# Performance work log

Hardware: AMD Instinct MI355X
Metric: run time of the kernel (lower is better)

Reference implementation:

```python
import jax, jax.numpy as jnp
import numpy as np


def _per_qubit_unitary(theta):
    # theta: [L, Nq, 3] float -> combined per-qubit 2x2 unitary [Nq, 2, 2] complex64
    # Circuit applies, for each layer l (l=0 first): RZ(theta[l,i,0]) -> RY(theta[l,i,1]) -> RZ(theta[l,i,2])
    half = theta.astype(jnp.float32) * 0.5

    def rz(p):  # p: [Nq] -> [Nq,2,2]
        e = jnp.exp(-1j * p)  # complex64
        z = jnp.zeros_like(e)
        return jnp.stack([jnp.stack([e, z], -1), jnp.stack([z, jnp.conj(e)], -1)], -2)

    def ry(p):  # p: [Nq] -> [Nq,2,2]
        c, s = jnp.cos(p), jnp.sin(p)
        return jnp.stack([jnp.stack([c, -s], -1), jnp.stack([s, c], -1)], -2).astype(jnp.complex64)

    n_layers, n_qubits = theta.shape[0], theta.shape[1]
    U = jnp.broadcast_to(jnp.eye(2, dtype=jnp.complex64), (n_qubits, 2, 2))
    for l in range(n_layers):  # small fixed layer loop
        Ul = rz(half[l, :, 2]) @ ry(half[l, :, 1]) @ rz(half[l, :, 0])
        U = Ul @ U
    return U


def _vqc_state(angles, theta):
    # angles: [B,S,Nq]; theta: [L,Nq,3] -> real part of 2^Nq state vector, [B,S,2^Nq]
    half = angles * 0.5
    # RY(a)|0> = cos(a/2)|0> + sin(a/2)|1>
    v = jnp.stack([jnp.cos(half), jnp.sin(half)], -1).astype(jnp.complex64)  # [B,S,Nq,2]
    U = _per_qubit_unitary(theta)  # [Nq,2,2]
    v = jnp.einsum('nij,bsnj->bsni', U, v)  # apply layered single-qubit unitaries
    # Kron across qubits; PennyLane wire 0 is most significant -> left-to-right kron
    state = v[:, :, 0, :]  # [B,S,2]
    n_qubits = v.shape[2]
    for q in range(1, n_qubits):  # small fixed qubit loop
        state = (state[..., :, None] * v[:, :, q][..., None, :])
        state = state.reshape(state.shape[0], state.shape[1], -1)
    return jnp.real(state)


def setup_inputs() -> dict:
    key = jax.random.key(0)
    k0, k1, k2, k3 = jax.random.split(key, 4)
    B, S, NQ, L = 8, 512, 12, 4
    return {
        'angles': jax.random.normal(k0, (B, S, NQ), dtype=jnp.float32),
        'theta_Q': jax.random.normal(k1, (L, NQ, 3), dtype=jnp.float32),
        'theta_K': jax.random.normal(k2, (L, NQ, 3), dtype=jnp.float32),
        'theta_V': jax.random.normal(k3, (L, NQ, 3), dtype=jnp.float32),
    }


def reference(angles, theta_Q, theta_K, theta_V):
    psi_Q = _vqc_state(angles, theta_Q)
    psi_K = _vqc_state(angles, theta_K)
    psi_V = _vqc_state(angles, theta_V)
    return (psi_Q, psi_K, psi_V)
```

## Files before the change

### kernel.cpp

```cpp
#include <hip/hip_runtime.h>


#define BS_TOTAL 4096
#define NQ 12
#define NL 4
#define NSTATE 4096

__device__ __forceinline__ float2 cmul(float2 a, float2 b) {
    return make_float2(a.x * b.x - a.y * b.y, a.x * b.y + a.y * b.x);
}
__device__ __forceinline__ float2 cconj(float2 a) { return make_float2(a.x, -a.y); }
__device__ __forceinline__ float2 cadd(float2 a, float2 b) { return make_float2(a.x + b.x, a.y + b.y); }

__global__ void build_U(const float* __restrict__ tQ, const float* __restrict__ tK,
                        const float* __restrict__ tV, float2* __restrict__ Uout) {
    int t = threadIdx.x;
    if (t >= 36) return;
    int m = t / NQ, n = t % NQ;
    const float* th = (m == 0) ? tQ : (m == 1) ? tK : tV;
    float2 U00 = {1.f, 0.f}, U01 = {0.f, 0.f}, U10 = {0.f, 0.f}, U11 = {1.f, 0.f};
    for (int l = 0; l < NL; ++l) {
        float c = 0.5f * th[(l * NQ + n) * 3 + 0];
        float b = 0.5f * th[(l * NQ + n) * 3 + 1];
        float a = 0.5f * th[(l * NQ + n) * 3 + 2];
        float sa, ca, sb, cb, sc, cc;
        sincosf(a, &sa, &ca);
        sincosf(b, &sb, &cb);
        sincosf(c, &sc, &cc);
        float2 ea = {ca, -sa};
        float2 ec = {cc, -sc};
        float2 p  = cmul(ea, ec);
        float2 q  = cmul(ea, cconj(ec));
        float2 A00 = { cb * p.x,  cb * p.y};
        float2 A01 = {-sb * q.x, -sb * q.y};
        float2 A10 = { sb * q.x, -sb * q.y};
        float2 A11 = { cb * p.x, -cb * p.y};
        float2 n00 = cadd(cmul(A00, U00), cmul(A01, U10));
        float2 n01 = cadd(cmul(A00, U01), cmul(A01, U11));
        float2 n10 = cadd(cmul(A10, U00), cmul(A11, U10));
        float2 n11 = cadd(cmul(A10, U01), cmul(A11, U11));
        U00 = n00; U01 = n01; U10 = n10; U11 = n11;
    }
    float2* o = Uout + (m * NQ + n) * 4;
    o[0] = U00; o[1] = U01; o[2] = U10; o[3] = U11;
}

__global__ __launch_bounds__(256) void vqc_state_kernel(
    const float* __restrict__ angles,
    const float2* __restrict__ U,
    float* __restrict__ out)
{
    const int bs = blockIdx.x;
    const int t  = threadIdx.x;

    __shared__ float  cs[NQ][2];
    __shared__ float2 vv[3][NQ][2];
    __shared__ float2 AB[3][2][16];
    __shared__ float2 Plo[3][16];
    __shared__ float2 Phi[3][256];

    if (t < NQ) {
        float a = angles[bs * NQ + t];
        float s, c;
        sincosf(0.5f * a, &s, &c);
        cs[t][0] = c; cs[t][1] = s;
    }
    __syncthreads();

    if (t < 36) {
        int m = t / NQ, n = t % NQ;
        float c = cs[n][0], s = cs[n][1];
        const float2* u = U + (m * NQ + n) * 4;
        float2 u00 = u[0], u01 = u[1], u10 = u[2], u11 = u[3];
        vv[m][n][0] = make_float2(u00.x * c + u01.x * s, u00.y * c + u01.y * s);
        vv[m][n][1] = make_float2(u10.x * c + u11.x * s, u10.y * c + u11.y * s);
    }
    __syncthreads();

    if (t < 144) {
        int m = t / 48, r = t % 48, g = r / 16, idx = r % 16;
        int q0 = g * 4;
        float2 p = cmul(cmul(vv[m][q0    ][(idx >> 3) & 1],
                             vv[m][q0 + 1][(idx >> 2) & 1]),
                        cmul(vv[m][q0 + 2][(idx >> 1) & 1],
                             vv[m][q0 + 3][ idx       & 1]));
        if (g < 2) AB[m][g][idx] = p; else Plo[m][idx] = p;
    }
    __syncthreads();

#pragma unroll
    for (int m = 0; m < 3; ++m)
        Phi[m][t] = cmul(AB[m][0][t >> 4], AB[m][1][t & 15]);
    __syncthreads();

    const int lobase = 4 * (t & 3);
    const int hsub   = t >> 2;
#pragma unroll
    for (int m = 0; m < 3; ++m) {
        float2 l0 = Plo[m][lobase + 0];
        float2 l1 = Plo[m][lobase + 1];
        float2 l2 = Plo[m][lobase + 2];
        float2 l3 = Plo[m][lobase + 3];
        float* po = out + (size_t)m * BS_TOTAL * NSTATE + (size_t)bs * NSTATE;
#pragma unroll
        for (int j = 0; j < 4; ++j) {
            float2 h = Phi[m][j * 64 + hsub];
            float4 r;
            r.x = h.x * l0.x - h.y * l0.y;
            r.y = h.x * l1.x - h.y * l1.y;
            r.z = h.x * l2.x - h.y * l2.y;
            r.w = h.x * l3.x - h.y * l3.y;
            *(float4*)(po + j * 1024 + t * 4) = r;
        }
    }
}

extern "C" void kernel_launch(void* const* d_in, const int* in_sizes, int n_in,
                              void* d_out, int out_size, void* d_ws, size_t ws_size,
                              hipStream_t stream) {
    (void)in_sizes; (void)n_in; (void)out_size; (void)ws_size;
    const float* angles = (const float*)d_in[0];
    const float* tQ     = (const float*)d_in[1];
    const float* tK     = (const float*)d_in[2];
    const float* tV     = (const float*)d_in[3];
    float2* Uws = (float2*)d_ws;

    build_U<<<1, 64, 0, stream>>>(tQ, tK, tV, Uws);
    vqc_state_kernel<<<BS_TOTAL, 256, 0, stream>>>(angles, Uws, (float*)d_out);
}
```

Baseline: 202.4 us.

## Fuse U construction into state kernel, process two samples per block, nontemporal stores

Removes the separate single-block build_U launch by having each block recompute the per-qubit unitaries in shared memory, which runs in parallel with the angle sincos. Each block now handles two (b,s) samples, halving the grid and amortizing the setup phases. Output writes use nontemporal vector stores to avoid polluting cache on the write-only 200MB output. The cost is redundant U computation in every block and more shared memory per block.

```diff
diff --git a/kernel.cpp b/kernel.cpp
--- a/kernel.cpp
+++ b/kernel.cpp
@@ -5,6 +5,9 @@
 #define NQ 12
 #define NL 4
 #define NSTATE 4096
+#define SPB 2
+
+typedef float vfloat4 __attribute__((ext_vector_type(4)));
 
 __device__ __forceinline__ float2 cmul(float2 a, float2 b) {
     return make_float2(a.x * b.x - a.y * b.y, a.x * b.y + a.y * b.x);
@@ -12,105 +15,110 @@
 __device__ __forceinline__ float2 cconj(float2 a) { return make_float2(a.x, -a.y); }
 __device__ __forceinline__ float2 cadd(float2 a, float2 b) { return make_float2(a.x + b.x, a.y + b.y); }
 
-__global__ void build_U(const float* __restrict__ tQ, const float* __restrict__ tK,
-                        const float* __restrict__ tV, float2* __restrict__ Uout) {
-    int t = threadIdx.x;
-    if (t >= 36) return;
-    int m = t / NQ, n = t % NQ;
-    const float* th = (m == 0) ? tQ : (m == 1) ? tK : tV;
-    float2 U00 = {1.f, 0.f}, U01 = {0.f, 0.f}, U10 = {0.f, 0.f}, U11 = {1.f, 0.f};
-    for (int l = 0; l < NL; ++l) {
-        float c = 0.5f * th[(l * NQ + n) * 3 + 0];
-        float b = 0.5f * th[(l * NQ + n) * 3 + 1];
-        float a = 0.5f * th[(l * NQ + n) * 3 + 2];
-        float sa, ca, sb, cb, sc, cc;
-        sincosf(a, &sa, &ca);
-        sincosf(b, &sb, &cb);
-        sincosf(c, &sc, &cc);
-        float2 ea = {ca, -sa};
-        float2 ec = {cc, -sc};
-        float2 p  = cmul(ea, ec);
-        float2 q  = cmul(ea, cconj(ec));
-        float2 A00 = { cb * p.x,  cb * p.y};
-        float2 A01 = {-sb * q.x, -sb * q.y};
-        float2 A10 = { sb * q.x, -sb * q.y};
-        float2 A11 = { cb * p.x, -cb * p.y};
-        float2 n00 = cadd(cmul(A00, U00), cmul(A01, U10));
-        float2 n01 = cadd(cmul(A00, U01), cmul(A01, U11));
-        float2 n10 = cadd(cmul(A10, U00), cmul(A11, U10));
-        float2 n11 = cadd(cmul(A10, U01), cmul(A11, U11));
-        U00 = n00; U01 = n01; U10 = n10; U11 = n11;
-    }
-    float2* o = Uout + (m * NQ + n) * 4;
-    o[0] = U00; o[1] = U01; o[2] = U10; o[3] = U11;
-}
-
-__global__ __launch_bounds__(256) void vqc_state_kernel(
+__global__ __launch_bounds__(256) void vqc_fused_kernel(
     const float* __restrict__ angles,
-    const float2* __restrict__ U,
+    const float* __restrict__ tQ,
+    const float* __restrict__ tK,
+    const float* __restrict__ tV,
     float* __restrict__ out)
 {
-    const int bs = blockIdx.x;
-    const int t  = threadIdx.x;
+    const int bs0 = blockIdx.x * SPB;
+    const int t   = threadIdx.x;
 
-    __shared__ float  cs[NQ][2];
-    __shared__ float2 vv[3][NQ][2];
-    __shared__ float2 AB[3][2][16];
-    __shared__ float2 Plo[3][16];
-    __shared__ float2 Phi[3][256];
+    __shared__ float2 Uu[3][NQ][4];
+    __shared__ float  cs[SPB][NQ][2];
+    __shared__ float2 vv[SPB][3][NQ][2];
+    __shared__ float2 AB[SPB][3][2][16];
+    __shared__ float2 Plo[SPB][3][16];
+    __shared__ float2 Phi[SPB][3][256];
 
-    if (t < NQ) {
-        float a = angles[bs * NQ + t];
+    if (t < 36) {
+        int m = t / NQ, n = t % NQ;
+        const float* th = (m == 0) ? tQ : (m == 1) ? tK : tV;
+        float2 U00 = {1.f, 0.f}, U01 = {0.f, 0.f}, U10 = {0.f, 0.f}, U11 = {1.f, 0.f};
+#pragma unroll
+        for (int l = 0; l < NL; ++l) {
+            float c = 0.5f * th[(l * NQ + n) * 3 + 0];
+            float b = 0.5f * th[(l * NQ + n) * 3 + 1];
+            float a = 0.5f * th[(l * NQ + n) * 3 + 2];
+            float sa, ca, sb, cb, sc, cc;
+            sincosf(a, &sa, &ca);
+            sincosf(b, &sb, &cb);
+            sincosf(c, &sc, &cc);
+            float2 ea = {ca, -sa};
+            float2 ec = {cc, -sc};
+            float2 p  = cmul(ea, ec);
+            float2 q  = cmul(ea, cconj(ec));
+            float2 A00 = { cb * p.x,  cb * p.y};
+            float2 A01 = {-sb * q.x, -sb * q.y};
+            float2 A10 = { sb * q.x, -sb * q.y};
+            float2 A11 = { cb * p.x, -cb * p.y};
+            float2 n00 = cadd(cmul(A00, U00), cmul(A01, U10));
+            float2 n01 = cadd(cmul(A00, U01), cmul(A01, U11));
+            float2 n10 = cadd(cmul(A10, U00), cmul(A11, U10));
+            float2 n11 = cadd(cmul(A10, U01), cmul(A11, U11));
+            U00 = n00; U01 = n01; U10 = n10; U11 = n11;
+        }
+        Uu[m][n][0] = U00; Uu[m][n][1] = U01; Uu[m][n][2] = U10; Uu[m][n][3] = U11;
+    } else if (t >= 64 && t < 64 + SPB * NQ) {
+        int idx = t - 64, s2 = idx / NQ, n = idx % NQ;
+        float a = angles[(bs0 + s2) * NQ + n];
         float s, c;
         sincosf(0.5f * a, &s, &c);
-        cs[t][0] = c; cs[t][1] = s;
+        cs[s2][n][0] = c; cs[s2][n][1] = s;
     }
     __syncthreads();
 
-    if (t < 36) {
-        int m = t / NQ, n = t % NQ;
-        float c = cs[n][0], s = cs[n][1];
-        const float2* u = U + (m * NQ + n) * 4;
-        float2 u00 = u[0], u01 = u[1], u10 = u[2], u11 = u[3];
-        vv[m][n][0] = make_float2(u00.x * c + u01.x * s, u00.y * c + u01.y * s);
-        vv[m][n][1] = make_float2(u10.x * c + u11.x * s, u10.y * c + u11.y * s);
-    }
-    __syncthreads();
-
-    if (t < 144) {
-        int m = t / 48, r = t % 48, g = r / 16, idx = r % 16;
-        int q0 = g * 4;
-        float2 p = cmul(cmul(vv[m][q0    ][(idx >> 3) & 1],
-                             vv[m][q0 + 1][(idx >> 2) & 1]),
-                        cmul(vv[m][q0 + 2][(idx >> 1) & 1],
-                             vv[m][q0 + 3][ idx       & 1]));
-        if (g < 2) AB[m][g][idx] = p; else Plo[m][idx] = p;
+    if (t < SPB * 36) {
+        int s2 = t / 36, r = t % 36, m = r / NQ, n = r % NQ;
+        float c = cs[s2][n][0], s = cs[s2][n][1];
+        float2 u00 = Uu[m][n][0], u01 = Uu[m][n][1], u10 = Uu[m][n][2], u11 = Uu[m][n][3];
+        vv[s2][m][n][0] = make_float2(u00.x * c + u01.x * s, u00.y * c + u01.y * s);
+        vv[s2][m][n][1] = make_float2(u10.x * c + u11.x * s, u10.y * c + u11.y * s);
     }
     __syncthreads();
 
 #pragma unroll
-    for (int m = 0; m < 3; ++m)
-        Phi[m][t] = cmul(AB[m][0][t >> 4], AB[m][1][t & 15]);
+    for (int task = t; task < SPB * 144; task += 256) {
+        int s2 = task / 144, r = task % 144, m = r / 48, g = (r % 48) / 16, idx = r % 16;
+        int q0 = g * 4;
+        float2 p = cmul(cmul(vv[s2][m][q0    ][(idx >> 3) & 1],
+                             vv[s2][m][q0 + 1][(idx >> 2) & 1]),
+                        cmul(vv[s2][m][q0 + 2][(idx >> 1) & 1],
+                             vv[s2][m][q0 + 3][ idx       & 1]));
+        if (g < 2) AB[s2][m][g][idx] = p; else Plo[s2][m][idx] = p;
+    }
+    __syncthreads();
+
+#pragma unroll
+    for (int i = 0; i < 6; ++i) {
+        int task = t + i * 256;
+        int s2 = task / 768, r = task % 768, m = r / 256, e = r % 256;
+        Phi[s2][m][e] = cmul(AB[s2][m][0][e >> 4], AB[s2][m][1][e & 15]);
+    }
     __syncthreads();
 
     const int lobase = 4 * (t & 3);
     const int hsub   = t >> 2;
 #pragma unroll
-    for (int m = 0; m < 3; ++m) {
-        float2 l0 = Plo[m][lobase + 0];
-        float2 l1 = Plo[m][lobase + 1];
-        float2 l2 = Plo[m][lobase + 2];
-        float2 l3 = Plo[m][lobase + 3];
-        float* po = out + (size_t)m * BS_TOTAL * NSTATE + (size_t)bs * NSTATE;
+    for (int s2 = 0; s2 < SPB; ++s2) {
 #pragma unroll
-        for (int j = 0; j < 4; ++j) {
-            float2 h = Phi[m][j * 64 + hsub];
-            float4 r;
-            r.x = h.x * l0.x - h.y * l0.y;
-            r.y = h.x * l1.x - h.y * l1.y;
-            r.z = h.x * l2.x - h.y * l2.y;
-            r.w = h.x * l3.x - h.y * l3.y;
-            *(float4*)(po + j * 1024 + t * 4) = r;
+        for (int m = 0; m < 3; ++m) {
+            float2 l0 = Plo[s2][m][lobase + 0];
+            float2 l1 = Plo[s2][m][lobase + 1];
+            float2 l2 = Plo[s2][m][lobase + 2];
+            float2 l3 = Plo[s2][m][lobase + 3];
+            float* po = out + (size_t)m * BS_TOTAL * NSTATE + (size_t)(bs0 + s2) * NSTATE;
+#pragma unroll
+            for (int j = 0; j < 4; ++j) {
+                float2 h = Phi[s2][m][j * 64 + hsub];
+                vfloat4 r;
+                r.x = h.x * l0.x - h.y * l0.y;
+                r.y = h.x * l1.x - h.y * l1.y;
+                r.z = h.x * l2.x - h.y * l2.y;
+                r.w = h.x * l3.x - h.y * l3.y;
+                __builtin_nontemporal_store(r, (vfloat4*)(po + j * 1024 + t * 4));
+            }
         }
     }
 }
@@ -118,13 +126,11 @@
 extern "C" void kernel_launch(void* const* d_in, const int* in_sizes, int n_in,
                               void* d_out, int out_size, void* d_ws, size_t ws_size,
                               hipStream_t stream) {
-    (void)in_sizes; (void)n_in; (void)out_size; (void)ws_size;
+    (void)in_sizes; (void)n_in; (void)out_size; (void)d_ws; (void)ws_size;
     const float* angles = (const float*)d_in[0];
     const float* tQ     = (const float*)d_in[1];
     const float* tK     = (const float*)d_in[2];
     const float* tV     = (const float*)d_in[3];
-    float2* Uws = (float2*)d_ws;
 
-    build_U<<<1, 64, 0, stream>>>(tQ, tK, tV, Uws);
-    vqc_state_kernel<<<BS_TOTAL, 256, 0, stream>>>(angles, Uws, (float*)d_out);
+    vqc_fused_kernel<<<BS_TOTAL / SPB, 256, 0, stream>>>(angles, tQ, tK, tV, (float*)d_out);
 }
```

Result: slower. 208.5 us (+3.0%).
